# Optimization experiments

Measured on AMD Instinct MI355X. Metric: run time of the kernel, lower is better.

The kernel has to match this reference:

```python
import jax, jax.numpy as jnp
import numpy as np

N, E = 50000, 800000
IN_DIM, HIDDEN, LATENT = 128, 256, 64


def setup_inputs() -> dict:
    key = jax.random.key(0)
    ks = jax.random.split(key, 10)
    def lin(k, fan_in, fan_out):
        s = 1.0 / np.sqrt(fan_in)
        return jax.random.uniform(k, (fan_in, fan_out), jnp.float32, -s, s)
    x = jax.random.normal(ks[0], (N, IN_DIM), jnp.float32)
    edge_index = jax.random.randint(ks[1], (2, E), 0, N, jnp.int64)
    return {
        "x": x,
        "edge_index": edge_index,
        # enc1: SAGEConv(in_dim, hidden): lin_l (neighbors, with bias), lin_r (root, no bias)
        "W1l": lin(ks[2], IN_DIM, HIDDEN),
        "b1": jnp.zeros((HIDDEN,), jnp.float32),
        "W1r": lin(ks[3], IN_DIM, HIDDEN),
        # enc2: SAGEConv(hidden, latent)
        "W2l": lin(ks[4], HIDDEN, LATENT),
        "b2": jnp.zeros((LATENT,), jnp.float32),
        "W2r": lin(ks[5], HIDDEN, LATENT),
        # decoder Linear(latent, in_dim)
        "Wd": lin(ks[6], LATENT, IN_DIM),
        "bd": jax.random.uniform(ks[7], (IN_DIM,), jnp.float32, -1.0 / np.sqrt(LATENT), 1.0 / np.sqrt(LATENT)),
    }


def _sage_conv(x, src, dst, Wl, b, Wr, num_nodes):
    # PyG SAGEConv (aggr='mean'): out = lin_l(mean_{j in N(i)} x_j) + lin_r(x_i)
    summed = jax.ops.segment_sum(x[src], dst, num_segments=num_nodes)   # [N, d]
    cnt = jax.ops.segment_sum(jnp.ones((src.shape[0],), x.dtype), dst, num_segments=num_nodes)
    mean = summed / jnp.maximum(cnt, 1.0)[:, None]
    return mean @ Wl + b + x @ Wr


def reference(x, edge_index, W1l, b1, W1r, W2l, b2, W2r, Wd, bd):
    src, dst = edge_index[0], edge_index[1]
    n = x.shape[0]
    h = jax.nn.relu(_sage_conv(x, src, dst, W1l, b1, W1r, n))
    z = _sage_conv(h, src, dst, W2l, b2, W2r, n)
    x_hat = z @ Wd + bd
    return (z, x_hat)
```

## Files before the change

kernel.cpp:

```cpp
#include <hip/hip_runtime.h>
#include <stdint.h>

#define NN 50000
#define NE 800000
#define NB 196
#define NBK 196
#define NBUK 196
#define CHK 4096
#define MTOT (NBUK * NBK)
#define MSB 151
#define CVTB 6250
#define PREPB 418

typedef __bf16 bf16x8 __attribute__((ext_vector_type(8)));
typedef float f32x4 __attribute__((ext_vector_type(4)));
typedef unsigned short ushort_t;
typedef unsigned short us4v __attribute__((ext_vector_type(4)));
typedef float f4v __attribute__((ext_vector_type(4)));

__device__ inline float bf2f(uint16_t u) {
    union { uint32_t i; float f; } v; v.i = ((uint32_t)u) << 16; return v.f;
}
__device__ inline uint16_t f2bf(float f) {
    uint32_t u = __float_as_uint(f);
    u += 0x7fffu + ((u >> 16) & 1u);
    return (uint16_t)(u >> 16);
}
__device__ inline float rdf(const void* p, int i, int bf) {
    return bf ? bf2f(((const ushort_t*)p)[i]) : ((const float*)p)[i];
}

__device__ inline int blk_or(int v, int* flag) {
    if (threadIdx.x == 0) *flag = 0;
    __syncthreads();
    if (v) atomicOr(flag, 1);
    __syncthreads();
    return *flag;
}
__device__ inline int detect_sh(const int* __restrict__ ei, int* flag) {
    int t = threadIdx.x;
    int v = ei[2 * t + 1] | ei[2 * (t + 256) + 1] | ei[2 * (t + 512) + 1] | ei[2 * (t + 768) + 1];
    return blk_or(v, flag) ? 0 : 1;
}
__device__ inline int detect_bf(const ushort_t* __restrict__ xw, int* flag) {
    int t = threadIdx.x;
    int bad = 0;
#pragma unroll
    for (int r = 0; r < 2; ++r) {
        uint16_t w = xw[t + 256 * r];
        int e = (w >> 7) & 0xFF;
        if (!(w == 0 || (e >= 96 && e <= 144))) bad = 1;
    }
    return blk_or(bad, flag) ? 0 : 1;
}

__global__ __launch_bounds__(256) void k_stage1(const int* __restrict__ ei, const void* __restrict__ x,
                                                const void* __restrict__ W1l, const void* __restrict__ W1r,
                                                const void* __restrict__ W2l, const void* __restrict__ W2r,
                                                const void* __restrict__ Wd,
                                                const void* __restrict__ b1, const void* __restrict__ b2,
                                                const void* __restrict__ bd,
                                                int* __restrict__ cntm, ushort_t* __restrict__ xb,
                                                ushort_t* __restrict__ wt, ushort_t* __restrict__ w2lt,
                                                ushort_t* __restrict__ w2rt, ushort_t* __restrict__ wdt,
                                                float* __restrict__ b1f, float* __restrict__ b2f,
                                                float* __restrict__ bdf) {
    __shared__ int flag;
    int b = blockIdx.x, t = threadIdx.x;
    if (b < NBK) {
        int sh = detect_sh(ei, &flag);
        __shared__ int hist[NBUK];
        if (t < NBUK) hist[t] = 0;
        __syncthreads();
        for (int i = t; i < CHK; i += 256) {
            int e = b * CHK + i;
            if (e < NE) {
                int d = ei[(size_t)(NE + e) << sh];
                atomicAdd(&hist[d >> 8], 1);
            }
        }
        __syncthreads();
        if (t < NBUK) cntm[t * NBK + b] = hist[t];
    } else if (b < NBK + CVTB) {
        int bf = detect_bf((const ushort_t*)x, &flag);
        int i = (b - NBK) * 256 + t;
        if (bf) {
            us4v v = __builtin_nontemporal_load(reinterpret_cast<const us4v*>(x) + i);
            *(reinterpret_cast<us4v*>(xb) + i) = v;
        } else {
            f4v v = __builtin_nontemporal_load(reinterpret_cast<const f4v*>(x) + i);
            us4v o;
            o.x = f2bf(v.x); o.y = f2bf(v.y); o.z = f2bf(v.z); o.w = f2bf(v.w);
            *(reinterpret_cast<us4v*>(xb) + i) = o;
        }
    } else {
        int bf = detect_bf((const ushort_t*)x, &flag);
        int idx = (b - NBK - CVTB) * 256 + t;
        if (idx < 65536) {
            int c = idx >> 8, k = idx & 255;
            float v = (k < 128) ? rdf(W1l, k * 256 + c, bf) : rdf(W1r, (k - 128) * 256 + c, bf);
            wt[c * 256 + k] = f2bf(v);
        } else if (idx < 81920) {
            int t2 = idx - 65536;
            int c = t2 >> 8, k = t2 & 255;
            w2lt[c * 256 + k] = f2bf(rdf(W2l, k * 64 + c, bf));
        } else if (idx < 98304) {
            int t2 = idx - 81920;
            int c = t2 >> 8, k = t2 & 255;
            w2rt[c * 256 + k] = f2bf(rdf(W2r, k * 64 + c, bf));
        } else if (idx < 106496) {
            int t2 = idx - 98304;
            int c = t2 >> 6, k = t2 & 63;
            wdt[c * 64 + k] = f2bf(rdf(Wd, k * 128 + c, bf));
        } else if (idx < 106752) {
            b1f[idx - 106496] = rdf(b1, idx - 106496, bf);
        } else if (idx < 106816) {
            b2f[idx - 106752] = rdf(b2, idx - 106752, bf);
        } else if (idx < 106944) {
            bdf[idx - 106816] = rdf(bd, idx - 106816, bf);
        }
    }
}

__device__ inline int block_scan256(int v, int* ws, int* btot) {
    int lane = threadIdx.x & 63, wv = threadIdx.x >> 6;
    int incl = v;
#pragma unroll
    for (int d = 1; d < 64; d <<= 1) {
        int n = __shfl_up(incl, d);
        if (lane >= d) incl += n;
    }
    if (lane == 63) ws[wv] = incl;
    __syncthreads();
    if (threadIdx.x == 0) {
        int r = 0;
#pragma unroll
        for (int k = 0; k < 4; ++k) { int t = ws[k]; ws[k] = r; r += t; }
        *btot = r;
    }
    __syncthreads();
    return ws[wv] + incl - v;
}

__global__ __launch_bounds__(256) void k_scanMA(const int* __restrict__ cntm, int* __restrict__ offm,
                                                int* __restrict__ bsM) {
    __shared__ int ws[4]; __shared__ int btot;
    int i = blockIdx.x * 256 + threadIdx.x;
    int v = (i < MTOT) ? cntm[i] : 0;
    int excl = block_scan256(v, ws, &btot);
    if (i < MTOT) offm[i] = excl;
    if (threadIdx.x == 0) bsM[blockIdx.x] = btot;
}

__device__ inline void bsm_prefix(const int* __restrict__ bsM, int* bsPre, int* ws, int* btot) {
    int t = threadIdx.x;
    int v = (t < MSB) ? bsM[t] : 0;
    int excl = block_scan256(v, ws, &btot[0]);
    bsPre[t] = excl;
    __syncthreads();
}

__global__ __launch_bounds__(256) void k_scatterC(const int* __restrict__ ei,
                                                  const int* __restrict__ offm, const int* __restrict__ bsM,
                                                  uint32_t* __restrict__ pairs) {
    __shared__ int cur[NBUK];
    __shared__ int bsPre[256];
    __shared__ int ws[4]; __shared__ int btot;
    __shared__ int flag;
    int t = threadIdx.x, blk = blockIdx.x;
    int sh = detect_sh(ei, &flag);
    bsm_prefix(bsM, bsPre, ws, &btot);
    if (t < NBUK) {
        int g = t * NBK + blk;
        cur[t] = offm[g] + bsPre[g >> 8];
    }
    __syncthreads();
    for (int i = t; i < CHK; i += 256) {
        int e = blk * CHK + i;
        if (e < NE) {
            int s = ei[(size_t)e << sh];
            int d = ei[(size_t)(NE + e) << sh];
            int pos = atomicAdd(&cur[d >> 8], 1);
            pairs[pos] = (uint32_t)s | ((uint32_t)(d & 255) << 16);
        }
    }
}

__global__ __launch_bounds__(256) void k_d12(const uint32_t* __restrict__ pairs, const int* __restrict__ offm,
                                             const int* __restrict__ bsM,
                                             int* __restrict__ rowptr, ushort_t* __restrict__ srclist) {
    __shared__ int hist[256];
    __shared__ int cur[256];
    __shared__ int bsPre[256];
    __shared__ int ws[4]; __shared__ int btot;
    int t = threadIdx.x, b = blockIdx.x;
    bsm_prefix(bsM, bsPre, ws, &btot);
    __shared__ int sbeg, send;
    if (t == 0) {
        int g0 = b * NBK;
        sbeg = offm[g0] + bsPre[g0 >> 8];
        if (b + 1 < NBUK) {
            int g1 = (b + 1) * NBK;
            send = offm[g1] + bsPre[g1 >> 8];
        } else {
            send = NE;
        }
    }
    hist[t] = 0;
    __syncthreads();
    int beg = sbeg, end = send;
    for (int i = beg + t; i < end; i += 256) {
        uint32_t p = pairs[i];
        atomicAdd(&hist[p >> 16], 1);
    }
    __syncthreads();
    int v = hist[t];
    int excl = block_scan256(v, ws, &btot);
    int node = b * 256 + t;
    int rp = beg + excl;
    if (node < NN) rowptr[node] = rp;
    cur[t] = rp;
    if (b == 0 && t == 0) rowptr[NN] = NE;
    __syncthreads();
    for (int i = beg + t; i < end; i += 256) {
        uint32_t p = pairs[i];
        int pos = atomicAdd(&cur[p >> 16], 1);
        srclist[pos] = (ushort_t)(p & 0xffff);
    }
}

__global__ __launch_bounds__(256) void k_agg128(const ushort_t* __restrict__ xb, const int* __restrict__ rowptr,
                                                const ushort_t* __restrict__ srclist, ushort_t* __restrict__ out) {
    int node = (blockIdx.x * 256 + threadIdx.x) >> 6;
    int lane = threadIdx.x & 63;
    if (node >= NN) return;
    int half = lane >> 5, l32 = lane & 31;
    int beg = rowptr[node], end = rowptr[node + 1];
    float a0 = 0.f, a1 = 0.f, a2 = 0.f, a3 = 0.f;
    int j = beg + half;
    for (; j + 14 < end; j += 16) {
        ushort4 p[8];
#pragma unroll
        for (int u = 0; u < 8; ++u) {
            int s = srclist[j + 2 * u];
            p[u] = *reinterpret_cast<const ushort4*>(xb + (size_t)s * 128 + l32 * 4);
        }
#pragma unroll
        for (int u = 0; u < 8; ++u) {
            a0 += bf2f(p[u].x); a1 += bf2f(p[u].y); a2 += bf2f(p[u].z); a3 += bf2f(p[u].w);
        }
    }
    for (; j + 6 < end; j += 8) {
        ushort4 p[4];
#pragma unroll
        for (int u = 0; u < 4; ++u) {
            int s = srclist[j + 2 * u];
            p[u] = *reinterpret_cast<const ushort4*>(xb + (size_t)s * 128 + l32 * 4);
        }
#pragma unroll
        for (int u = 0; u < 4; ++u) {
            a0 += bf2f(p[u].x); a1 += bf2f(p[u].y); a2 += bf2f(p[u].z); a3 += bf2f(p[u].w);
        }
    }
    for (; j < end; j += 2) {
        int s = srclist[j];
        ushort4 p = *reinterpret_cast<const ushort4*>(xb + (size_t)s * 128 + l32 * 4);
        a0 += bf2f(p.x); a1 += bf2f(p.y); a2 += bf2f(p.z); a3 += bf2f(p.w);
    }
    a0 += __shfl_xor(a0, 32);
    a1 += __shfl_xor(a1, 32);
    a2 += __shfl_xor(a2, 32);
    a3 += __shfl_xor(a3, 32);
    if (half == 0) {
        float inv = 1.0f / (float)max(end - beg, 1);
        ushort4 o;
        o.x = f2bf(a0 * inv); o.y = f2bf(a1 * inv); o.z = f2bf(a2 * inv); o.w = f2bf(a3 * inv);
        *reinterpret_cast<ushort4*>(out + (size_t)node * 128 + l32 * 4) = o;
    }
}

__global__ __launch_bounds__(256, 2) void k_gemm12(const ushort_t* __restrict__ meanx, const ushort_t* __restrict__ xb,
                                                   const ushort_t* __restrict__ wt, const float* __restrict__ b1f,
                                                   const ushort_t* __restrict__ w2lt, const ushort_t* __restrict__ w2rt,
                                                   const float* __restrict__ b2f,
                                                   ushort_t* __restrict__ y, float* __restrict__ r) {
    __shared__ alignas(16) ushort_t ht[16 * 256];
    int wv = threadIdx.x >> 6, lane = threadIdx.x & 63;
    int m = lane & 15, q = lane >> 4;
    bf16x8 B1[8][4];
#pragma unroll
    for (int ks = 0; ks < 8; ++ks) {
        int kb = ks * 32 + q * 8;
#pragma unroll
        for (int ct = 0; ct < 4; ++ct)
            B1[ks][ct] = *reinterpret_cast<const bf16x8*>(wt + (size_t)(wv * 64 + ct * 16 + m) * 256 + kb);
    }
    int op = wv >> 1;
    int cb = (wv & 1) * 32;
    const ushort_t* wtx = op ? w2rt : w2lt;
    bf16x8 B2[8][2];
#pragma unroll
    for (int ks = 0; ks < 8; ++ks) {
        int kb = ks * 32 + q * 8;
#pragma unroll
        for (int ct = 0; ct < 2; ++ct)
            B2[ks][ct] = *reinterpret_cast<const bf16x8*>(wtx + (size_t)(cb + ct * 16 + m) * 256 + kb);
    }
    float bias2[2];
#pragma unroll
    for (int ct = 0; ct < 2; ++ct) bias2[ct] = b2f[cb + ct * 16 + m];

    const int ntiles = NN / 16;
    for (int t = blockIdx.x; t < ntiles; t += gridDim.x) {
        int r0 = t * 16;
        int row = r0 + m;
        f32x4 acc[4];
#pragma unroll
        for (int ct = 0; ct < 4; ++ct) acc[ct] = (f32x4){0.f, 0.f, 0.f, 0.f};
#pragma unroll
        for (int ks = 0; ks < 8; ++ks) {
            int kb = ks * 32 + q * 8;
            const ushort_t* ap = (ks < 4) ? (meanx + (size_t)row * 128 + kb)
                                          : (xb + (size_t)row * 128 + (kb - 128));
            bf16x8 a = *reinterpret_cast<const bf16x8*>(ap);
#pragma unroll
            for (int ct = 0; ct < 4; ++ct)
                acc[ct] = __builtin_amdgcn_mfma_f32_16x16x32_bf16(a, B1[ks][ct], acc[ct], 0, 0, 0);
        }
#pragma unroll
        for (int ct = 0; ct < 4; ++ct) {
            int c = wv * 64 + ct * 16 + m;
            float bias = b1f[c];
#pragma unroll
            for (int i = 0; i < 4; ++i) {
                int lr = q * 4 + i;
                int off = (lr * 512 + c * 2) ^ ((lr & 7) << 4);
                *reinterpret_cast<ushort_t*>(reinterpret_cast<char*>(ht) + off) =
                    f2bf(fmaxf(acc[ct][i] + bias, 0.f));
            }
        }
        __syncthreads();
        f32x4 acc2[2];
        acc2[0] = (f32x4){0.f, 0.f, 0.f, 0.f}; acc2[1] = acc2[0];
#pragma unroll
        for (int ks = 0; ks < 8; ++ks) {
            int boff = (m * 512 + ks * 64 + q * 16) ^ ((m & 7) << 4);
            bf16x8 a = *reinterpret_cast<const bf16x8*>(reinterpret_cast<const char*>(ht) + boff);
#pragma unroll
            for (int ct = 0; ct < 2; ++ct)
                acc2[ct] = __builtin_amdgcn_mfma_f32_16x16x32_bf16(a, B2[ks][ct], acc2[ct], 0, 0, 0);
        }
#pragma unroll
        for (int ct = 0; ct < 2; ++ct) {
            int c = cb + ct * 16 + m;
#pragma unroll
            for (int i = 0; i < 4; ++i) {
                int rr = r0 + q * 4 + i;
                if (op == 0) y[(size_t)rr * 64 + c] = f2bf(acc2[ct][i]);
                else         r[(size_t)rr * 64 + c] = acc2[ct][i] + bias2[ct];
            }
        }
        __syncthreads();
    }
}

__global__ __launch_bounds__(256) void k_agg2g3(const ushort_t* __restrict__ y, const int* __restrict__ rowptr,
                                                const ushort_t* __restrict__ srclist,
                                                float* zr,
                                                const ushort_t* __restrict__ wdt, const float* __restrict__ bdf,
                                                float* __restrict__ xhat) {
    __shared__ alignas(16) ushort_t zt[16][72];
    int b = blockIdx.x;
    int wv = threadIdx.x >> 6, lane = threadIdx.x & 63;
    int m = lane & 15, q = lane >> 4;
    bf16x8 B[2][2];
#pragma unroll
    for (int ks = 0; ks < 2; ++ks) {
        int kb = ks * 32 + q * 8;
#pragma unroll
        for (int ct = 0; ct < 2; ++ct)
            B[ks][ct] = *reinterpret_cast<const bf16x8*>(wdt + (size_t)(wv * 32 + ct * 16 + m) * 64 + kb);
    }
    float bias0 = bdf[wv * 32 + m], bias1 = bdf[wv * 32 + 16 + m];

    int quarter = lane >> 4, l16 = lane & 15;
#pragma unroll
    for (int s = 0; s < 4; ++s) {
        int node = b * 16 + wv * 4 + s;
        int beg = rowptr[node], end = rowptr[node + 1];
        float a0 = 0.f, a1 = 0.f, a2 = 0.f, a3 = 0.f;
        int j = beg + quarter;
        for (; j + 12 < end; j += 16) {
            ushort4 p[4];
#pragma unroll
            for (int u = 0; u < 4; ++u) {
                int sx = srclist[j + 4 * u];
                p[u] = *reinterpret_cast<const ushort4*>(y + (size_t)sx * 64 + l16 * 4);
            }
#pragma unroll
            for (int u = 0; u < 4; ++u) {
                a0 += bf2f(p[u].x); a1 += bf2f(p[u].y); a2 += bf2f(p[u].z); a3 += bf2f(p[u].w);
            }
        }
        for (; j < end; j += 4) {
            int sx = srclist[j];
            ushort4 p = *reinterpret_cast<const ushort4*>(y + (size_t)sx * 64 + l16 * 4);
            a0 += bf2f(p.x); a1 += bf2f(p.y); a2 += bf2f(p.z); a3 += bf2f(p.w);
        }
        a0 += __shfl_xor(a0, 16); a0 += __shfl_xor(a0, 32);
        a1 += __shfl_xor(a1, 16); a1 += __shfl_xor(a1, 32);
        a2 += __shfl_xor(a2, 16); a2 += __shfl_xor(a2, 32);
        a3 += __shfl_xor(a3, 16); a3 += __shfl_xor(a3, 32);
        if (quarter == 0) {
            float inv = 1.0f / (float)max(end - beg, 1);
            float4 rv = *reinterpret_cast<const float4*>(zr + (size_t)node * 64 + l16 * 4);
            f4v zo;
            zo.x = a0 * inv + rv.x;
            zo.y = a1 * inv + rv.y;
            zo.z = a2 * inv + rv.z;
            zo.w = a3 * inv + rv.w;
            __builtin_nontemporal_store(zo, reinterpret_cast<f4v*>(zr + (size_t)node * 64 + l16 * 4));
            uint2 o;
            o.x = (uint32_t)f2bf(zo.x) | ((uint32_t)f2bf(zo.y) << 16);
            o.y = (uint32_t)f2bf(zo.z) | ((uint32_t)f2bf(zo.w) << 16);
            *reinterpret_cast<uint2*>(&zt[wv * 4 + s][l16 * 4]) = o;
        }
    }
    __syncthreads();
    f32x4 acc[2];
    acc[0] = (f32x4){0.f, 0.f, 0.f, 0.f}; acc[1] = acc[0];
#pragma unroll
    for (int ks = 0; ks < 2; ++ks) {
        bf16x8 a = *reinterpret_cast<const bf16x8*>(&zt[m][ks * 32 + q * 8]);
#pragma unroll
        for (int ct = 0; ct < 2; ++ct)
            acc[ct] = __builtin_amdgcn_mfma_f32_16x16x32_bf16(a, B[ks][ct], acc[ct], 0, 0, 0);
    }
#pragma unroll
    for (int ct = 0; ct < 2; ++ct) {
        int c = wv * 32 + ct * 16 + m;
        float bb = ct ? bias1 : bias0;
#pragma unroll
        for (int i = 0; i < 4; ++i) {
            int rr = b * 16 + q * 4 + i;
            __builtin_nontemporal_store(acc[ct][i] + bb, &xhat[(size_t)rr * 128 + c]);
        }
    }
}

extern "C" void kernel_launch(void* const* d_in, const int* in_sizes, int n_in,
                              void* d_out, int out_size, void* d_ws, size_t ws_size,
                              hipStream_t stream) {
    const void *px = nullptr, *pei = nullptr, *pW1l = nullptr, *pW1r = nullptr,
               *pW2l = nullptr, *pW2r = nullptr, *pWd = nullptr,
               *pb1 = nullptr, *pb2 = nullptr, *pbd = nullptr;
    for (int i = 0; i < n_in; ++i) {
        const void* p = d_in[i];
        switch (in_sizes[i]) {
            case 6400000: px  = p; break;
            case 1600000: pei = p; break;
            case 32768:   if (!pW1l) pW1l = p; else pW1r = p; break;
            case 16384:   if (!pW2l) pW2l = p; else pW2r = p; break;
            case 8192:    pWd = p; break;
            case 256:     pb1 = p; break;
            case 128:     pbd = p; break;
            case 64:      pb2 = p; break;
            default: break;
        }
    }
    if (!px || !pei || !pW1l || !pW1r || !pW2l || !pW2r || !pWd || !pb1 || !pb2 || !pbd) {
        px = d_in[0]; pei = d_in[1]; pW1l = d_in[2]; pb1 = d_in[3]; pW1r = d_in[4];
        pW2l = d_in[5]; pb2 = d_in[6]; pW2r = d_in[7]; pWd = d_in[8]; pbd = d_in[9];
    }
    const int* ei = (const int*)pei;

    char* base = (char*)d_ws;
    size_t off = 0;
    auto alloc = [&](size_t bytes) -> void* {
        void* r = base + off;
        off = (off + bytes + 255) & ~(size_t)255;
        return r;
    };
    int* rowptr   = (int*)alloc((size_t)(NN + 1) * 4);
    int* cntm     = (int*)alloc((size_t)MTOT * 4);
    int* offm     = (int*)alloc((size_t)MTOT * 4);
    int* bsM      = (int*)alloc(256 * 4);
    uint32_t* pairs = (uint32_t*)alloc((size_t)NE * 4);
    ushort_t* srclist = (ushort_t*)alloc((size_t)NE * 2);
    ushort_t* wt   = (ushort_t*)alloc((size_t)65536 * 2);
    ushort_t* w2lt = (ushort_t*)alloc((size_t)16384 * 2);
    ushort_t* w2rt = (ushort_t*)alloc((size_t)16384 * 2);
    ushort_t* wdt  = (ushort_t*)alloc((size_t)8192 * 2);
    float* b1f    = (float*)alloc(256 * 4);
    float* b2f    = (float*)alloc(64 * 4);
    float* bdf    = (float*)alloc(128 * 4);
    ushort_t* xb  = (ushort_t*)alloc((size_t)NN * 128 * 2);
    ushort_t* y   = (ushort_t*)alloc((size_t)NN * 64 * 2);

    float* out_z    = (float*)d_out;
    float* out_xhat = out_z + (size_t)NN * 64;

    ushort_t* meanx = (ushort_t*)out_xhat;
    float*    rbuf  = out_z;

    k_stage1<<<NBK + CVTB + PREPB, 256, 0, stream>>>(ei, px, pW1l, pW1r, pW2l, pW2r, pWd, pb1, pb2, pbd,
                                                     cntm, xb, wt, w2lt, w2rt, wdt, b1f, b2f, bdf);

    k_scanMA<<<MSB, 256, 0, stream>>>(cntm, offm, bsM);
    k_scatterC<<<NBK, 256, 0, stream>>>(ei, offm, bsM, pairs);
    k_d12<<<NBUK, 256, 0, stream>>>(pairs, offm, bsM, rowptr, srclist);

    int ab = (NN + 3) / 4;
    k_agg128<<<ab, 256, 0, stream>>>(xb, rowptr, srclist, meanx);

    k_gemm12<<<512, 256, 0, stream>>>(meanx, xb, wt, b1f, w2lt, w2rt, b2f, y, rbuf);
    k_agg2g3<<<NN / 16, 256, 0, stream>>>(y, rowptr, srclist, rbuf, wdt, bdf, out_xhat);
}
```

Before: 220.4 us.

## Fold count-matrix scan into scatter and bucket kernels, widen aggregation unroll

Removes the separate k_scanMA launch. The scatter and bucket-sort kernels now compute their bucket offsets directly: each block redundantly sums rows of the 196x196 count matrix and runs a block scan. This drops one kernel launch and the offm/bsM intermediate buffers, at the cost of every block reading about 38K counts with strided row loads. A 32-wide unrolled loop is also added in the first-layer aggregation, putting more gathers in flight for high-degree nodes at the cost of extra registers.

```diff
diff --git a/kernel.cpp b/kernel.cpp
--- a/kernel.cpp
+++ b/kernel.cpp
@@ -8,7 +8,6 @@
 #define NBUK 196
 #define CHK 4096
 #define MTOT (NBUK * NBK)
-#define MSB 151
 #define CVTB 6250
 #define PREPB 418
 
@@ -142,38 +141,24 @@
     return ws[wv] + incl - v;
 }
 
-__global__ __launch_bounds__(256) void k_scanMA(const int* __restrict__ cntm, int* __restrict__ offm,
-                                                int* __restrict__ bsM) {
-    __shared__ int ws[4]; __shared__ int btot;
-    int i = blockIdx.x * 256 + threadIdx.x;
-    int v = (i < MTOT) ? cntm[i] : 0;
-    int excl = block_scan256(v, ws, &btot);
-    if (i < MTOT) offm[i] = excl;
-    if (threadIdx.x == 0) bsM[blockIdx.x] = btot;
-}
-
-__device__ inline void bsm_prefix(const int* __restrict__ bsM, int* bsPre, int* ws, int* btot) {
-    int t = threadIdx.x;
-    int v = (t < MSB) ? bsM[t] : 0;
-    int excl = block_scan256(v, ws, &btot[0]);
-    bsPre[t] = excl;
-    __syncthreads();
-}
-
-__global__ __launch_bounds__(256) void k_scatterC(const int* __restrict__ ei,
-                                                  const int* __restrict__ offm, const int* __restrict__ bsM,
+__global__ __launch_bounds__(256) void k_scatterC(const int* __restrict__ ei, const int* __restrict__ cntm,
                                                   uint32_t* __restrict__ pairs) {
     __shared__ int cur[NBUK];
-    __shared__ int bsPre[256];
     __shared__ int ws[4]; __shared__ int btot;
     __shared__ int flag;
     int t = threadIdx.x, blk = blockIdx.x;
     int sh = detect_sh(ei, &flag);
-    bsm_prefix(bsM, bsPre, ws, &btot);
+    int rowsum = 0, part = 0;
     if (t < NBUK) {
-        int g = t * NBK + blk;
-        cur[t] = offm[g] + bsPre[g >> 8];
-    }
+        const int* row = cntm + t * NBK;
+        for (int b2 = 0; b2 < NBK; ++b2) {
+            int c = row[b2];
+            rowsum += c;
+            if (b2 < blk) part += c;
+        }
+    }
+    int bpre = block_scan256(rowsum, ws, &btot);
+    if (t < NBUK) cur[t] = bpre + part;
     __syncthreads();
     for (int i = t; i < CHK; i += 256) {
         int e = blk * CHK + i;
@@ -186,29 +171,25 @@
     }
 }
 
-__global__ __launch_bounds__(256) void k_d12(const uint32_t* __restrict__ pairs, const int* __restrict__ offm,
-                                             const int* __restrict__ bsM,
+__global__ __launch_bounds__(256) void k_d12(const uint32_t* __restrict__ pairs, const int* __restrict__ cntm,
                                              int* __restrict__ rowptr, ushort_t* __restrict__ srclist) {
     __shared__ int hist[256];
     __shared__ int cur[256];
-    __shared__ int bsPre[256];
+    __shared__ int bpreA[NBUK + 1];
     __shared__ int ws[4]; __shared__ int btot;
     int t = threadIdx.x, b = blockIdx.x;
-    bsm_prefix(bsM, bsPre, ws, &btot);
-    __shared__ int sbeg, send;
-    if (t == 0) {
-        int g0 = b * NBK;
-        sbeg = offm[g0] + bsPre[g0 >> 8];
-        if (b + 1 < NBUK) {
-            int g1 = (b + 1) * NBK;
-            send = offm[g1] + bsPre[g1 >> 8];
-        } else {
-            send = NE;
-        }
-    }
+    int rowsum = 0;
+    if (t < NBUK) {
+        const int* row = cntm + t * NBK;
+        for (int b2 = 0; b2 < NBK; ++b2) rowsum += row[b2];
+    }
+    int bpre = block_scan256(rowsum, ws, &btot);
+    if (t < NBUK) bpreA[t] = bpre;
+    if (t == NBUK - 1) bpreA[NBUK] = bpre + rowsum;
     hist[t] = 0;
     __syncthreads();
-    int beg = sbeg, end = send;
+    int beg = bpreA[b];
+    int end = bpreA[b + 1];
     for (int i = beg + t; i < end; i += 256) {
         uint32_t p = pairs[i];
         atomicAdd(&hist[p >> 16], 1);
@@ -238,6 +219,18 @@
     int beg = rowptr[node], end = rowptr[node + 1];
     float a0 = 0.f, a1 = 0.f, a2 = 0.f, a3 = 0.f;
     int j = beg + half;
+    for (; j + 30 < end; j += 32) {
+        ushort4 p[16];
+#pragma unroll
+        for (int u = 0; u < 16; ++u) {
+            int s = srclist[j + 2 * u];
+            p[u] = *reinterpret_cast<const ushort4*>(xb + (size_t)s * 128 + l32 * 4);
+        }
+#pragma unroll
+        for (int u = 0; u < 16; ++u) {
+            a0 += bf2f(p[u].x); a1 += bf2f(p[u].y); a2 += bf2f(p[u].z); a3 += bf2f(p[u].w);
+        }
+    }
     for (; j + 14 < end; j += 16) {
         ushort4 p[8];
 #pragma unroll
@@ -483,8 +476,6 @@
     };
     int* rowptr   = (int*)alloc((size_t)(NN + 1) * 4);
     int* cntm     = (int*)alloc((size_t)MTOT * 4);
-    int* offm     = (int*)alloc((size_t)MTOT * 4);
-    int* bsM      = (int*)alloc(256 * 4);
     uint32_t* pairs = (uint32_t*)alloc((size_t)NE * 4);
     ushort_t* srclist = (ushort_t*)alloc((size_t)NE * 2);
     ushort_t* wt   = (ushort_t*)alloc((size_t)65536 * 2);
@@ -506,9 +497,8 @@
     k_stage1<<<NBK + CVTB + PREPB, 256, 0, stream>>>(ei, px, pW1l, pW1r, pW2l, pW2r, pWd, pb1, pb2, pbd,
                                                      cntm, xb, wt, w2lt, w2rt, wdt, b1f, b2f, bdf);
 
-    k_scanMA<<<MSB, 256, 0, stream>>>(cntm, offm, bsM);
-    k_scatterC<<<NBK, 256, 0, stream>>>(ei, offm, bsM, pairs);
-    k_d12<<<NBUK, 256, 0, stream>>>(pairs, offm, bsM, rowptr, srclist);
+    k_scatterC<<<NBK, 256, 0, stream>>>(ei, cntm, pairs);
+    k_d12<<<NBUK, 256, 0, stream>>>(pairs, cntm, rowptr, srclist);
 
     int ab = (NN + 3) / 4;
     k_agg128<<<ab, 256, 0, stream>>>(xb, rowptr, srclist, meanx);
```

Measured after the change: 226.0 us. +2.5%, slower.
